# Kernel optimization log

Hardware: AMD Instinct MI355X
Metric: run time of the kernel (lower is better)

## Reference

```python
import jax, jax.numpy as jnp
import numpy as np

H, W, C, CLS, R, B = 32, 32, 512, 1000, 64, 128

def setup_inputs() -> dict:
    key = jax.random.key(0)
    k = jax.random.split(key, 6)
    return {
        "x":   jax.random.normal(k[0], (B, C, W, H), dtype=jnp.float32),
        "U1":  jax.random.normal(k[1], (H, R),  dtype=jnp.float32) * 0.1,
        "U2":  jax.random.normal(k[2], (W, R),  dtype=jnp.float32) * 0.1,
        "U3":  jax.random.normal(k[3], (C, R),  dtype=jnp.float32) * 0.1,
        "U4":  jax.random.normal(k[4], (CLS, R), dtype=jnp.float32) * 0.1,
        "lam": jax.random.normal(k[5], (R,),    dtype=jnp.float32) * 0.1,
    }

def reference(x, U1, U2, U3, U4, lam):
    # Original: T[cls,c,w,h] = sum_r lam[r] U4[cls,r] U3[c,r] U2[w,r] U1[h,r]
    # then out[b,cls] = sum_{c,w,h} x[b,c,w,h] * T[cls,c,w,h].
    # Equivalent fused contraction (never materializes the dense CP tensor):
    t = jnp.einsum('bcwh,hr->bcwr', x, U1)      # contract h
    t = jnp.einsum('bcwr,wr->bcr', t, U2)       # contract w
    t = jnp.einsum('bcr,cr->br', t, U3)         # contract c
    out = jnp.einsum('br,r,Cr->bC', t, lam, U4) # scale by lam, expand classes
    return out
```

## Files before the change

kernel.cpp:

```cpp
#include <hip/hip_runtime.h>
#include <stdint.h>

#define HH 32
#define WW 32
#define CC 512
#define CLS 1000
#define RR 64
#define BB 128
#define KK 1024
#define MM (BB*CC)

#define KSPLIT 4
#define KS (KK/KSPLIT)
#define QS (KS/32)

typedef __bf16  bf16x8 __attribute__((ext_vector_type(8)));
typedef float   f32x4  __attribute__((ext_vector_type(4)));
typedef uint32_t u32x4 __attribute__((ext_vector_type(4)));

__global__ void prep_v(const float* __restrict__ U1, const float* __restrict__ U2,
                       __bf16* __restrict__ Vf) {
    int idx = blockIdx.x * 256 + threadIdx.x;
    int l  = idx & 63;
    int qf = idx >> 6;
    int f  = qf & 3;
    int q  = qf >> 2;
    int n  = f * 16 + (l & 15);
    int kb = q * 32 + (l >> 4) * 8;
#pragma unroll
    for (int j = 0; j < 8; ++j) {
        int k = kb + j;
        int w = k >> 5, h = k & 31;
        float v = U2[w * RR + n] * U1[h * RR + n];
        Vf[(size_t)idx * 8 + j] = (__bf16)v;
    }
}

__global__ void __launch_bounds__(256)
main_k(const float* __restrict__ x, const __bf16* __restrict__ Vf,
       const float* __restrict__ U3, float* __restrict__ t3) {
    __shared__ alignas(16) __bf16 vs[QS * 4 * 64 * 8];
    __shared__ float red[4][64];

    {
        const u32x4* src = (const u32x4*)(Vf + (size_t)blockIdx.y * QS * 4 * 64 * 8);
        u32x4* dst = (u32x4*)vs;
#pragma unroll
        for (int i = 0; i < 8; ++i)
            dst[threadIdx.x + i * 256] = src[threadIdx.x + i * 256];
    }
    __syncthreads();

    const int tid = threadIdx.x;
    const int wv  = tid >> 6;
    const int l   = tid & 63;
    const int m   = blockIdx.x * 64 + wv * 16 + (l & 15);
    const int k0  = blockIdx.y * KS;

    const float* xp = x + (size_t)m * KK + k0 + ((l >> 4) * 8);

    f32x4 acc[4] = {};

#pragma unroll
    for (int q = 0; q < QS; ++q) {
        f32x4 a0 = *(const f32x4*)(xp + q * 32);
        f32x4 a1 = *(const f32x4*)(xp + q * 32 + 4);
        bf16x8 af;
        af[0] = (__bf16)a0.x; af[1] = (__bf16)a0.y;
        af[2] = (__bf16)a0.z; af[3] = (__bf16)a0.w;
        af[4] = (__bf16)a1.x; af[5] = (__bf16)a1.y;
        af[6] = (__bf16)a1.z; af[7] = (__bf16)a1.w;
#pragma unroll
        for (int f = 0; f < 4; ++f) {
            bf16x8 bf = ((const bf16x8*)vs)[(q * 4 + f) * 64 + l];
            acc[f] = __builtin_amdgcn_mfma_f32_16x16x32_bf16(af, bf, acc[f], 0, 0, 0);
        }
    }

    const int b      = blockIdx.x >> 3;
    const int c_base = (blockIdx.x * 64) & (CC - 1);
    const int c_l    = c_base + wv * 16 + (l >> 4) * 4;

    float p[4];
#pragma unroll
    for (int f = 0; f < 4; ++f) {
        int r = f * 16 + (l & 15);
        float s = 0.f;
#pragma unroll
        for (int i = 0; i < 4; ++i)
            s += acc[f][i] * U3[(c_l + i) * RR + r];
        p[f] = s;
    }
#pragma unroll
    for (int f = 0; f < 4; ++f) {
        p[f] += __shfl_xor(p[f], 16, 64);
        p[f] += __shfl_xor(p[f], 32, 64);
    }
    if (l < 16) {
#pragma unroll
        for (int f = 0; f < 4; ++f) red[wv][f * 16 + l] = p[f];
    }
    __syncthreads();
    if (tid < 64) {
        float s = red[0][tid] + red[1][tid] + red[2][tid] + red[3][tid];
        atomicAdd(&t3[b * RR + tid], s);
    }
}

__global__ void out_k(const float* __restrict__ t3, const float* __restrict__ lam,
                      const float* __restrict__ U4, float* __restrict__ out) {
    __shared__ float sl[RR];
    const int b = blockIdx.y;
    const int tid = threadIdx.x;
    if (tid < RR) sl[tid] = t3[b * RR + tid] * lam[tid];
    __syncthreads();
    const int cls = blockIdx.x * 256 + tid;
    if (cls < CLS) {
        const f32x4* u4 = (const f32x4*)(U4 + (size_t)cls * RR);
        float s = 0.f;
#pragma unroll
        for (int i = 0; i < 16; ++i) {
            f32x4 v = u4[i];
            s += v.x * sl[i*4+0] + v.y * sl[i*4+1] + v.z * sl[i*4+2] + v.w * sl[i*4+3];
        }
        out[b * CLS + cls] = s;
    }
}

extern "C" void kernel_launch(void* const* d_in, const int* in_sizes, int n_in,
                              void* d_out, int out_size, void* d_ws, size_t ws_size,
                              hipStream_t stream) {
    const float* x   = (const float*)d_in[0];
    const float* U1  = (const float*)d_in[1];
    const float* U2  = (const float*)d_in[2];
    const float* U3  = (const float*)d_in[3];
    const float* U4  = (const float*)d_in[4];
    const float* lam = (const float*)d_in[5];

    __bf16* Vf = (__bf16*)d_ws;
    float*  t3 = (float*)((char*)d_ws + 128 * 1024);
    float*  out = (float*)d_out;

    hipMemsetAsync(t3, 0, BB * RR * sizeof(float), stream);
    prep_v<<<32, 256, 0, stream>>>(U1, U2, Vf);
    main_k<<<dim3(MM / 64, KSPLIT), 256, 0, stream>>>(x, Vf, U3, t3);
    out_k<<<dim3(4, BB), 256, 0, stream>>>(t3, lam, U4, out);
}
```

Baseline: 387.5 us.

## Fuse V-factor prep into main kernel and replace atomics with partial-sum buffer

Each main_k block now builds its bf16 slice of U2⊗U1 in shared memory directly from U1/U2, so the prep_v kernel and the workspace round-trip go away. The atomicAdd into t3 is replaced by per-block partial writes into a 32-slot buffer that out_k reduces, which also removes the memset launch. x loads become nontemporal and main_k gets a launch_bounds occupancy hint. The cost is that every block recomputes its V slice redundantly with strided scalar loads of U1/U2, and out_k has to read 32 partials per batch row.

```diff
diff --git a/kernel.cpp b/kernel.cpp
--- a/kernel.cpp
+++ b/kernel.cpp
@@ -16,55 +16,48 @@
 
 typedef __bf16  bf16x8 __attribute__((ext_vector_type(8)));
 typedef float   f32x4  __attribute__((ext_vector_type(4)));
-typedef uint32_t u32x4 __attribute__((ext_vector_type(4)));
 
-__global__ void prep_v(const float* __restrict__ U1, const float* __restrict__ U2,
-                       __bf16* __restrict__ Vf) {
-    int idx = blockIdx.x * 256 + threadIdx.x;
-    int l  = idx & 63;
-    int qf = idx >> 6;
-    int f  = qf & 3;
-    int q  = qf >> 2;
-    int n  = f * 16 + (l & 15);
-    int kb = q * 32 + (l >> 4) * 8;
-#pragma unroll
-    for (int j = 0; j < 8; ++j) {
-        int k = kb + j;
-        int w = k >> 5, h = k & 31;
-        float v = U2[w * RR + n] * U1[h * RR + n];
-        Vf[(size_t)idx * 8 + j] = (__bf16)v;
-    }
-}
-
-__global__ void __launch_bounds__(256)
-main_k(const float* __restrict__ x, const __bf16* __restrict__ Vf,
-       const float* __restrict__ U3, float* __restrict__ t3) {
+__global__ void __launch_bounds__(256, 4)
+main_k(const float* __restrict__ x, const float* __restrict__ U1,
+       const float* __restrict__ U2, const float* __restrict__ U3,
+       float* __restrict__ t3p) {
     __shared__ alignas(16) __bf16 vs[QS * 4 * 64 * 8];
     __shared__ float red[4][64];
 
-    {
-        const u32x4* src = (const u32x4*)(Vf + (size_t)blockIdx.y * QS * 4 * 64 * 8);
-        u32x4* dst = (u32x4*)vs;
+    const int tid = threadIdx.x;
+    const int k0  = blockIdx.y * KS;
+
 #pragma unroll
-        for (int i = 0; i < 8; ++i)
-            dst[threadIdx.x + i * 256] = src[threadIdx.x + i * 256];
+    for (int i = 0; i < 8; ++i) {
+        int idx = tid + i * 256;
+        int l  = idx & 63;
+        int qf = idx >> 6;
+        int f  = qf & 3;
+        int q  = qf >> 2;
+        int n  = f * 16 + (l & 15);
+        int kb = k0 + q * 32 + ((l >> 4) << 3);
+        int w  = kb >> 5;
+        int hb = kb & 31;
+        float u2 = U2[w * RR + n];
+        bf16x8 vv;
+#pragma unroll
+        for (int j = 0; j < 8; ++j)
+            vv[j] = (__bf16)(u2 * U1[(hb + j) * RR + n]);
+        ((bf16x8*)vs)[idx] = vv;
     }
     __syncthreads();
 
-    const int tid = threadIdx.x;
-    const int wv  = tid >> 6;
-    const int l   = tid & 63;
-    const int m   = blockIdx.x * 64 + wv * 16 + (l & 15);
-    const int k0  = blockIdx.y * KS;
-
+    const int wv = tid >> 6;
+    const int l  = tid & 63;
+    const int m  = blockIdx.x * 64 + wv * 16 + (l & 15);
     const float* xp = x + (size_t)m * KK + k0 + ((l >> 4) * 8);
 
     f32x4 acc[4] = {};
 
 #pragma unroll
     for (int q = 0; q < QS; ++q) {
-        f32x4 a0 = *(const f32x4*)(xp + q * 32);
-        f32x4 a1 = *(const f32x4*)(xp + q * 32 + 4);
+        f32x4 a0 = __builtin_nontemporal_load((const f32x4*)(xp + q * 32));
+        f32x4 a1 = __builtin_nontemporal_load((const f32x4*)(xp + q * 32 + 4));
         bf16x8 af;
         af[0] = (__bf16)a0.x; af[1] = (__bf16)a0.y;
         af[2] = (__bf16)a0.z; af[3] = (__bf16)a0.w;
@@ -103,27 +96,40 @@
     __syncthreads();
     if (tid < 64) {
         float s = red[0][tid] + red[1][tid] + red[2][tid] + red[3][tid];
-        atomicAdd(&t3[b * RR + tid], s);
+        int slot = ((blockIdx.x & 7) << 2) | blockIdx.y;
+        t3p[((size_t)b * 32 + slot) * RR + tid] = s;
     }
 }
 
-__global__ void out_k(const float* __restrict__ t3, const float* __restrict__ lam,
-                      const float* __restrict__ U4, float* __restrict__ out) {
+__global__ void __launch_bounds__(256)
+out_k(const float* __restrict__ t3p, const float* __restrict__ lam,
+      const float* __restrict__ U4, float* __restrict__ out) {
+    __shared__ float pr[4][RR];
     __shared__ float sl[RR];
-    const int b = blockIdx.y;
+    const int b   = blockIdx.y;
     const int tid = threadIdx.x;
-    if (tid < RR) sl[tid] = t3[b * RR + tid] * lam[tid];
+    const int r   = tid & 63, g = tid >> 6;
+
+    float s = 0.f;
+#pragma unroll
+    for (int i = 0; i < 8; ++i)
+        s += t3p[((size_t)b * 32 + g * 8 + i) * RR + r];
+    pr[g][r] = s;
     __syncthreads();
+    if (tid < RR)
+        sl[tid] = (pr[0][tid] + pr[1][tid] + pr[2][tid] + pr[3][tid]) * lam[tid];
+    __syncthreads();
+
     const int cls = blockIdx.x * 256 + tid;
     if (cls < CLS) {
         const f32x4* u4 = (const f32x4*)(U4 + (size_t)cls * RR);
-        float s = 0.f;
+        float sacc = 0.f;
 #pragma unroll
         for (int i = 0; i < 16; ++i) {
             f32x4 v = u4[i];
-            s += v.x * sl[i*4+0] + v.y * sl[i*4+1] + v.z * sl[i*4+2] + v.w * sl[i*4+3];
+            sacc += v.x * sl[i*4+0] + v.y * sl[i*4+1] + v.z * sl[i*4+2] + v.w * sl[i*4+3];
         }
-        out[b * CLS + cls] = s;
+        out[b * CLS + cls] = sacc;
     }
 }
 
@@ -137,12 +143,9 @@
     const float* U4  = (const float*)d_in[4];
     const float* lam = (const float*)d_in[5];
 
-    __bf16* Vf = (__bf16*)d_ws;
-    float*  t3 = (float*)((char*)d_ws + 128 * 1024);
-    float*  out = (float*)d_out;
+    float* t3p = (float*)d_ws;
+    float* out = (float*)d_out;
 
-    hipMemsetAsync(t3, 0, BB * RR * sizeof(float), stream);
-    prep_v<<<32, 256, 0, stream>>>(U1, U2, Vf);
-    main_k<<<dim3(MM / 64, KSPLIT), 256, 0, stream>>>(x, Vf, U3, t3);
-    out_k<<<dim3(4, BB), 256, 0, stream>>>(t3, lam, U4, out);
+    main_k<<<dim3(MM / 64, KSPLIT), 256, 0, stream>>>(x, U1, U2, U3, t3p);
+    out_k<<<dim3(4, BB), 256, 0, stream>>>(t3p, lam, U4, out);
 }
```

New measurement: 370.7 us. -4.4%, faster.
